# Kernel tuning notes

Measured on AMD Instinct MI355X. Metric: run time of the kernel, lower is better.

## Reference

```python
import jax, jax.numpy as jnp
import numpy as np

S = 16384   # total tokens (batch*seq flattened)
D = 1024    # model_dim
E = 32      # num_global_experts
H = 1024    # expert hidden size
CAP = 512   # capacity = capacity_factor * ceil(S / E)


def setup_inputs() -> dict:
    key = jax.random.key(0)
    k1, k2, k3, k4 = jax.random.split(key, 4)
    x = jax.random.normal(k1, (S, D), jnp.float32)
    wg = jax.random.normal(k2, (E, D), jnp.float32) * 0.02
    w1 = jax.random.normal(k3, (E, D, H), jnp.float32) * 0.02
    w2 = jax.random.normal(k4, (E, H, D), jnp.float32) * 0.02
    return {"x": x, "wg": wg, "w1": w1, "w2": w2}


def _moe_forward(x, wg, w1, w2):
    # --- Top1Gate ---
    logits = x @ wg.T                                   # [S, E]
    gates = jax.nn.softmax(logits, axis=1)              # [S, E]
    idx = jnp.argmax(logits, axis=1)                    # [S] int
    mask1 = jax.nn.one_hot(idx, E, dtype=jnp.int32)     # [S, E]
    gates1_s = jnp.sum(gates * mask1.astype(gates.dtype), axis=1)  # [S]
    # load-balance aux loss (fp32 path)
    me = jnp.sum(gates.astype(jnp.float32), axis=0)
    ce = jnp.sum(mask1.astype(jnp.float32), axis=0)
    l_loss = jnp.sum(me * ce) * (float(E) / float(S * S))
    # positions within expert (tutel cumsum_sub_one)
    loc = jnp.sum(jnp.cumsum(mask1, axis=0) * mask1, axis=1) - 1   # [S]
    valid = loc < CAP                                   # capacity drop
    slot = jnp.where(valid, idx * CAP + loc, 0)         # flat slot id, dropped -> 0 (masked below)

    # --- GatingEncoder: scatter tokens into [E*CAP, D] buffer ---
    xm = x * valid[:, None].astype(x.dtype)
    dispatched = jnp.zeros((E * CAP, D), x.dtype).at[slot].add(xm)
    dispatched = dispatched.reshape(E, CAP, D)

    # --- ExpertsGemm: per-expert FFN (world_size == 1, all-to-all is identity) ---
    h = jax.nn.relu(jnp.einsum('ecd,edh->ech', dispatched, w1))    # [E, CAP, H]
    expert_out = jnp.einsum('ech,ehd->ecd', h, w2).reshape(E * CAP, D)

    # --- GatingDecoder: gather back + weight by gate ---
    y = expert_out[slot] * (gates1_s * valid.astype(gates1_s.dtype))[:, None]
    return y, l_loss


def reference(x, wg, w1, w2):
    return _moe_forward(x, wg, w1, w2)
```

## Files before the change

kernel.cpp:

```cpp
#include <hip/hip_runtime.h>
#include <stdint.h>

static constexpr int nS   = 16384;
static constexpr int nD   = 1024;
static constexpr int nE   = 32;
static constexpr int nH   = 1024;
static constexpr int nCAP = 512;

static constexpr int GT = 64;
static constexpr int GB = nS / GT;

typedef __bf16 bf16x8 __attribute__((ext_vector_type(8)));
typedef float  f32x4  __attribute__((ext_vector_type(4)));
typedef unsigned short u16x8 __attribute__((ext_vector_type(8)));

static __device__ __forceinline__ unsigned short f2bf(float f) {
    __bf16 h = (__bf16)f;
    return __builtin_bit_cast(unsigned short, h);
}

static __device__ __forceinline__ void gload16(const void* g, void* l) {
    __builtin_amdgcn_global_load_lds(
        (const __attribute__((address_space(1))) void*)g,
        (__attribute__((address_space(3))) void*)l, 16, 0, 0);
}

__global__ __launch_bounds__(128) void k_gate(
    const float* __restrict__ x, const float* __restrict__ wg,
    unsigned short* __restrict__ xbf, int* __restrict__ idxo,
    float* __restrict__ gateval, int* __restrict__ counts,
    float* __restrict__ me_part)
{
    __shared__ float xs[GT][65];
    __shared__ float wgs[nE][65];
    __shared__ float gl[GT][nE + 1];
    __shared__ int   hist[nE];

    const int tid = threadIdx.x;
    const int tb  = blockIdx.x * GT;
    if (tid < nE) hist[tid] = 0;

    const int t0 = (tid >> 3) * 4;
    const int e0 = (tid & 7) * 4;
    float acc[4][4] = {};

    for (int ch = 0; ch < nD / 64; ++ch) {
#pragma unroll
        for (int i = 0; i < 4; ++i) {
            int f = tid + i * 128;
            int r = f >> 4, c4 = f & 15;
            const float4 v = *(const float4*)&wg[(size_t)r * nD + ch * 64 + c4 * 4];
            wgs[r][c4*4+0] = v.x; wgs[r][c4*4+1] = v.y;
            wgs[r][c4*4+2] = v.z; wgs[r][c4*4+3] = v.w;
        }
#pragma unroll
        for (int i = 0; i < 8; ++i) {
            int f = tid + i * 128;
            int r = f >> 4, c4 = f & 15;
            size_t go = (size_t)(tb + r) * nD + ch * 64 + c4 * 4;
            const float4 v = *(const float4*)&x[go];
            xs[r][c4*4+0] = v.x; xs[r][c4*4+1] = v.y;
            xs[r][c4*4+2] = v.z; xs[r][c4*4+3] = v.w;
            unsigned long long pk = (unsigned long long)f2bf(v.x)
                | ((unsigned long long)f2bf(v.y) << 16)
                | ((unsigned long long)f2bf(v.z) << 32)
                | ((unsigned long long)f2bf(v.w) << 48);
            *(unsigned long long*)&xbf[go] = pk;
        }
        __syncthreads();
#pragma unroll 4
        for (int k = 0; k < 64; ++k) {
            float xa[4], wb[4];
#pragma unroll
            for (int i = 0; i < 4; ++i) xa[i] = xs[t0 + i][k];
#pragma unroll
            for (int j = 0; j < 4; ++j) wb[j] = wgs[e0 + j][k];
#pragma unroll
            for (int i = 0; i < 4; ++i)
#pragma unroll
                for (int j = 0; j < 4; ++j) acc[i][j] += xa[i] * wb[j];
        }
        __syncthreads();
    }

#pragma unroll
    for (int i = 0; i < 4; ++i)
#pragma unroll
        for (int j = 0; j < 4; ++j) gl[t0 + i][e0 + j] = acc[i][j];
    __syncthreads();

    if (tid < GT) {
        float mx = gl[tid][0]; int bi = 0;
#pragma unroll
        for (int e = 1; e < nE; ++e) { float v = gl[tid][e]; if (v > mx) { mx = v; bi = e; } }
        float den = 0.f;
#pragma unroll
        for (int e = 0; e < nE; ++e) { float g = expf(gl[tid][e] - mx); gl[tid][e] = g; den += g; }
        float inv = 1.f / den;
#pragma unroll
        for (int e = 0; e < nE; ++e) gl[tid][e] *= inv;
        idxo[tb + tid] = bi;
        gateval[tb + tid] = inv;
        atomicAdd(&hist[bi], 1);
    }
    __syncthreads();
    if (tid < nE) {
        float s = 0.f;
        for (int t = 0; t < GT; ++t) s += gl[t][tid];
        me_part[blockIdx.x * nE + tid] = s;
        counts[blockIdx.x * nE + tid] = hist[tid];
    }
}

__global__ __launch_bounds__(1024) void k_scan(
    const int* __restrict__ counts, int* __restrict__ offsets,
    const float* __restrict__ me_part, float* __restrict__ loss_out,
    int* __restrict__ inv_slot)
{
    __shared__ int tot[nE];
    __shared__ float mesum[nE];
    const int w = threadIdx.x >> 6;
    const int lane = threadIdx.x & 63;
    for (int e = w; e < nE; e += 16) {
        int v[4]; int s = 0;
#pragma unroll
        for (int i = 0; i < 4; ++i) { v[i] = counts[(lane * 4 + i) * nE + e]; s += v[i]; }
        int incl = s;
#pragma unroll
        for (int d = 1; d < 64; d <<= 1) {
            int o = __shfl_up(incl, d);
            if (lane >= d) incl += o;
        }
        int run = incl - s;
#pragma unroll
        for (int i = 0; i < 4; ++i) { offsets[(lane * 4 + i) * nE + e] = run; run += v[i]; }
        int total = __shfl(incl, 63);
        if (lane == 0) tot[e] = total;

        float ms = 0.f;
#pragma unroll
        for (int i = 0; i < 4; ++i) ms += me_part[(lane * 4 + i) * nE + e];
#pragma unroll
        for (int d = 32; d >= 1; d >>= 1) ms += __shfl_xor(ms, d);
        if (lane == 0) mesum[e] = ms;
    }
    __syncthreads();
    if (threadIdx.x < 64) {
        float val = (threadIdx.x < nE) ? mesum[threadIdx.x] * (float)tot[threadIdx.x] : 0.f;
#pragma unroll
        for (int d = 32; d >= 1; d >>= 1) val += __shfl_xor(val, d);
        if (threadIdx.x == 0)
            *loss_out = val * ((float)nE / ((float)nS * (float)nS));
    }
    for (int i = threadIdx.x; i < nE * nCAP; i += 1024) {
        const int e = i >> 9, loc = i & (nCAP - 1);
        if (loc >= tot[e]) inv_slot[i] = -1;
    }
}

__global__ __launch_bounds__(64) void k_assign(
    const int* __restrict__ idxi, const int* __restrict__ offsets,
    int* __restrict__ inv_slot, float* __restrict__ y)
{
    __shared__ int drop[64];
    __shared__ int ndrop;
    const int lane = threadIdx.x;
    const int t = blockIdx.x * 64 + lane;
    const int e = idxi[t];
    if (lane == 0) ndrop = 0;
    __syncthreads();
    int rank = 0;
#pragma unroll
    for (int ee = 0; ee < nE; ++ee) {
        unsigned long long m = __ballot(e == ee);
        if (e == ee) rank = __popcll(m & ((1ull << lane) - 1ull));
    }
    const int loc = offsets[blockIdx.x * nE + e] + rank;
    if (loc < nCAP) {
        inv_slot[e * nCAP + loc] = t;
    } else {
        int p = atomicAdd(&ndrop, 1);
        drop[p] = t;
    }
    __syncthreads();
    const int nd = ndrop;
    for (int i = 0; i < nd; ++i) {
        const int tt = drop[i];
        float4 z = {0.f, 0.f, 0.f, 0.f};
        for (int c = lane; c < nD / 4; c += 64)
            *(float4*)&y[(size_t)tt * nD + c * 4] = z;
    }
}

__global__ __launch_bounds__(256) void k_transpose(
    const float* __restrict__ w1, const float* __restrict__ w2,
    unsigned short* __restrict__ w1t, unsigned short* __restrict__ w2t)
{
    __shared__ unsigned short T[64 * 258];
    const float* src = blockIdx.z ? w2 : w1;
    unsigned short* dst = blockIdx.z ? w2t : w1t;
    const int e    = blockIdx.y;
    const int dblk = blockIdx.x & 15;
    const int hblk = blockIdx.x >> 4;
    const int t = threadIdx.x;
    const int wv = t >> 6, lane = t & 63;

    const float* sbase = src + ((size_t)e * 1024 + dblk * 64) * 1024 + hblk * 256;

#pragma unroll
    for (int i = 0; i < 16; ++i) {
        const int d = i * 4 + wv;
        const float4 v = *(const float4*)&sbase[(size_t)d * 1024 + lane * 4];
        unsigned long long pk = (unsigned long long)f2bf(v.x)
            | ((unsigned long long)f2bf(v.y) << 16)
            | ((unsigned long long)f2bf(v.z) << 32)
            | ((unsigned long long)f2bf(v.w) << 48);
        *(unsigned long long*)&T[d * 258 + lane * 4] = pk;
    }
    __syncthreads();

    const size_t cbase0 = (((size_t)e * 8 + hblk * 2) * 16 + dblk) * 8192;
    const size_t cbase1 = cbase0 + 16 * 8192;
#pragma unroll
    for (int s = 0; s < 8; ++s) {
        const int off = s * 2048 + t * 8;
        const int hl  = off >> 6;
        const int k8  = off & 63;
        u16x8 v;
#pragma unroll
        for (int r = 0; r < 8; ++r) v[r] = T[(k8 + r) * 258 + hl];
        const size_t base = (off < 8192) ? cbase0 : cbase1;
        *(u16x8*)&dst[base + (off & 8191)] = v;
    }
}

template <int MODE>
__global__ __launch_bounds__(256) void k_gemm(
    const unsigned short* __restrict__ Abase,
    const unsigned short* __restrict__ Bt,
    const int* __restrict__ inv_slot,
    const float* __restrict__ gateval,
    unsigned short* __restrict__ hout,
    float* __restrict__ y)
{
    __shared__ __attribute__((aligned(16))) unsigned short As[128 * 64];
    __shared__ __attribute__((aligned(16))) unsigned short Bs[128 * 64];

    const int tid = threadIdx.x;
    const int lane = tid & 63, w = tid >> 6;
    const int n0 = blockIdx.x * 128, m0 = blockIdx.y * 128, e = blockIdx.z;

    const unsigned short* gA[4];
    const int j = lane & 7;
#pragma unroll
    for (int s = 0; s < 4; ++s) {
        const int cw = s * 4 + w;
        const int row = cw * 8 + (lane >> 3);
        if (MODE == 0) {
            int tok = inv_slot[e * nCAP + m0 + row];
            if (tok < 0) tok = 0;
            gA[s] = Abase + (size_t)tok * nD + j * 8;
        } else {
            gA[s] = Abase + ((size_t)e * nCAP + m0 + row) * nH + j * 8;
        }
    }
    const unsigned short* gB = Bt + (((size_t)e * 8 + (n0 >> 7)) * 16) * 8192
                             + (size_t)tid * 8;

    f32x4 acc[4][4];
#pragma unroll
    for (int a = 0; a < 4; ++a)
#pragma unroll
        for (int b = 0; b < 4; ++b) acc[a][b] = (f32x4){0.f, 0.f, 0.f, 0.f};

    const int wm = w >> 1, wn = w & 1;
    const int abyte = (wm * 64 + (lane & 15)) * 128 + (lane >> 4) * 16;
    const int bbyte = (wn * 64 + (lane & 15)) * 128 + (lane >> 4) * 16;

    for (int k0 = 0; k0 < 1024 / 64; ++k0) {
#pragma unroll
        for (int s = 0; s < 4; ++s) {
            gload16(gA[s] + k0 * 64, (char*)As + (s * 4 + w) * 1024);
            gload16(gB + (size_t)k0 * 8192 + ((s * 4 + w) * 512 + lane * 8 - tid * 8),
                    (char*)Bs + (s * 4 + w) * 1024);
        }
        __syncthreads();
#pragma unroll
        for (int kk = 0; kk < 2; ++kk) {
            bf16x8 a[4], b[4];
#pragma unroll
            for (int mi = 0; mi < 4; ++mi)
                a[mi] = *(const bf16x8*)((const char*)As + abyte + mi * 2048 + kk * 64);
#pragma unroll
            for (int ni = 0; ni < 4; ++ni)
                b[ni] = *(const bf16x8*)((const char*)Bs + bbyte + ni * 2048 + kk * 64);
#pragma unroll
            for (int mi = 0; mi < 4; ++mi)
#pragma unroll
                for (int ni = 0; ni < 4; ++ni)
                    acc[mi][ni] = __builtin_amdgcn_mfma_f32_16x16x32_bf16(
                        a[mi], b[ni], acc[mi][ni], 0, 0, 0);
        }
        __syncthreads();
    }

    const int col_l = lane & 15, rg = lane >> 4;
    if (MODE == 0) {
#pragma unroll
        for (int mi = 0; mi < 4; ++mi) {
#pragma unroll
            for (int ni = 0; ni < 4; ++ni) {
                const f32x4 v = acc[mi][ni];
                const int n = n0 + wn * 64 + ni * 16 + col_l;
#pragma unroll
                for (int r = 0; r < 4; ++r) {
                    const int m = m0 + wm * 64 + mi * 16 + rg * 4 + r;
                    const float f = v[r] > 0.f ? v[r] : 0.f;
                    hout[((size_t)e * nCAP + m) * nH + n] = f2bf(f);
                }
            }
        }
    } else {
#pragma unroll
        for (int mi = 0; mi < 4; ++mi) {
            int tok[4]; float gv[4];
#pragma unroll
            for (int r = 0; r < 4; ++r) {
                const int m = m0 + wm * 64 + mi * 16 + rg * 4 + r;
                tok[r] = inv_slot[e * nCAP + m];
                gv[r] = (tok[r] >= 0) ? gateval[tok[r]] : 0.f;
            }
#pragma unroll
            for (int ni = 0; ni < 4; ++ni) {
                const f32x4 v = acc[mi][ni];
                const int n = n0 + wn * 64 + ni * 16 + col_l;
#pragma unroll
                for (int r = 0; r < 4; ++r) {
                    if (tok[r] >= 0)
                        y[(size_t)tok[r] * nD + n] = v[r] * gv[r];
                }
            }
        }
    }
}

extern "C" void kernel_launch(void* const* d_in, const int* in_sizes, int n_in,
                              void* d_out, int out_size, void* d_ws, size_t ws_size,
                              hipStream_t stream) {
    const float* x  = (const float*)d_in[0];
    const float* wg = (const float*)d_in[1];
    const float* w1 = (const float*)d_in[2];
    const float* w2 = (const float*)d_in[3];
    float* y = (float*)d_out;
    float* loss = y + (size_t)nS * nD;

    char* ws = (char*)d_ws;
    unsigned short* w1t  = (unsigned short*)(ws);
    unsigned short* w2t  = (unsigned short*)(ws + (64ull << 20));
    unsigned short* hbuf = (unsigned short*)(ws + (128ull << 20));
    unsigned short* xbf  = (unsigned short*)(ws + (160ull << 20));
    char* p = ws + (192ull << 20);
    int*   idxb    = (int*)p;   p += (size_t)nS * 4;
    float* gateval = (float*)p; p += (size_t)nS * 4;
    int*   counts  = (int*)p;   p += (size_t)GB * nE * 4;
    int*   offsets = (int*)p;   p += (size_t)GB * nE * 4;
    float* me_part = (float*)p; p += (size_t)GB * nE * 4;
    int*   inv_slot= (int*)p;

    k_gate<<<GB, 128, 0, stream>>>(x, wg, xbf, idxb, gateval, counts, me_part);
    k_scan<<<1, 1024, 0, stream>>>(counts, offsets, me_part, loss, inv_slot);
    k_assign<<<GB, 64, 0, stream>>>(idxb, offsets, inv_slot, y);
    k_transpose<<<dim3(64, 32, 2), 256, 0, stream>>>(w1, w2, w1t, w2t);
    k_gemm<0><<<dim3(8, 4, 32), 256, 0, stream>>>(xbf, w1t, inv_slot, gateval, hbuf, y);
    k_gemm<1><<<dim3(8, 4, 32), 256, 0, stream>>>(hbuf, w2t, inv_slot, gateval, hbuf, y);
}
```

Measured before the change: 311.2 us.

## Stage GEMM epilogues through LDS for coalesced stores and remap blocks per XCD

Both GEMM epilogues now write the accumulator tile into shared memory first and then store it with 16-byte vectorized rows. Before, each thread issued scattered 2-byte (bf16) or 4-byte (fp32) stores. The y scatter in the second GEMM now writes contiguous float4 chunks per token row, done in two halves so the fp32 tile fits in LDS. Launch is flattened to 1024 blocks with a swizzled block-id so that consecutive blocks landing on the same XCD share an expert, which should improve L2 reuse of weights. The cost is extra LDS traffic and barriers in the epilogue.

Measured after the change: 312.0 us. About the same (+0.2%).

```diff
diff --git a/kernel.cpp b/kernel.cpp
--- a/kernel.cpp
+++ b/kernel.cpp
@@ -243,12 +243,14 @@
     unsigned short* __restrict__ hout,
     float* __restrict__ y)
 {
-    __shared__ __attribute__((aligned(16))) unsigned short As[128 * 64];
-    __shared__ __attribute__((aligned(16))) unsigned short Bs[128 * 64];
+    __shared__ __attribute__((aligned(16))) unsigned short SMEM[128 * 64 * 2];
+    unsigned short* As = SMEM;
+    unsigned short* Bs = SMEM + 128 * 64;
 
     const int tid = threadIdx.x;
     const int lane = tid & 63, w = tid >> 6;
-    const int n0 = blockIdx.x * 128, m0 = blockIdx.y * 128, e = blockIdx.z;
+    const int bid = (blockIdx.x & 7) * 128 + (blockIdx.x >> 3);
+    const int n0 = (bid & 7) * 128, m0 = ((bid >> 3) & 3) * 128, e = bid >> 5;
 
     const unsigned short* gA[4];
     const int j = lane & 7;
@@ -311,35 +313,56 @@
 #pragma unroll
             for (int ni = 0; ni < 4; ++ni) {
                 const f32x4 v = acc[mi][ni];
-                const int n = n0 + wn * 64 + ni * 16 + col_l;
+                const int nl = wn * 64 + ni * 16 + col_l;
 #pragma unroll
                 for (int r = 0; r < 4; ++r) {
-                    const int m = m0 + wm * 64 + mi * 16 + rg * 4 + r;
+                    const int ml = wm * 64 + mi * 16 + rg * 4 + r;
                     const float f = v[r] > 0.f ? v[r] : 0.f;
-                    hout[((size_t)e * nCAP + m) * nH + n] = f2bf(f);
+                    SMEM[ml * 128 + nl] = f2bf(f);
                 }
             }
         }
+        __syncthreads();
+#pragma unroll
+        for (int s = 0; s < 8; ++s) {
+            const int u = tid + s * 256;
+            const int row = u >> 4, nu = u & 15;
+            const u16x8 v = *(const u16x8*)((const char*)SMEM + u * 16);
+            *(u16x8*)&hout[((size_t)e * nCAP + m0 + row) * nH + n0 + nu * 8] = v;
+        }
     } else {
-#pragma unroll
-        for (int mi = 0; mi < 4; ++mi) {
-            int tok[4]; float gv[4];
-#pragma unroll
-            for (int r = 0; r < 4; ++r) {
-                const int m = m0 + wm * 64 + mi * 16 + rg * 4 + r;
-                tok[r] = inv_slot[e * nCAP + m];
-                gv[r] = (tok[r] >= 0) ? gateval[tok[r]] : 0.f;
-            }
-#pragma unroll
-            for (int ni = 0; ni < 4; ++ni) {
-                const f32x4 v = acc[mi][ni];
-                const int n = n0 + wn * 64 + ni * 16 + col_l;
-#pragma unroll
-                for (int r = 0; r < 4; ++r) {
-                    if (tok[r] >= 0)
-                        y[(size_t)tok[r] * nD + n] = v[r] * gv[r];
+        float* Lf = (float*)SMEM;
+#pragma unroll
+        for (int P = 0; P < 2; ++P) {
+            if (wm == P) {
+#pragma unroll
+                for (int mi = 0; mi < 4; ++mi) {
+#pragma unroll
+                    for (int ni = 0; ni < 4; ++ni) {
+                        const f32x4 v = acc[mi][ni];
+                        const int nl = wn * 64 + ni * 16 + col_l;
+#pragma unroll
+                        for (int r = 0; r < 4; ++r) {
+                            const int ml = mi * 16 + rg * 4 + r;
+                            Lf[ml * 128 + nl] = v[r];
+                        }
+                    }
                 }
             }
+            __syncthreads();
+#pragma unroll
+            for (int s = 0; s < 8; ++s) {
+                const int u = tid + s * 256;
+                const int row = u >> 5, f4 = u & 31;
+                const int tok = inv_slot[e * nCAP + m0 + P * 64 + row];
+                if (tok >= 0) {
+                    const float gv = gateval[tok];
+                    float4 v = *(const float4*)((const char*)SMEM + u * 16);
+                    v.x *= gv; v.y *= gv; v.z *= gv; v.w *= gv;
+                    *(float4*)&y[(size_t)tok * nD + n0 + f4 * 4] = v;
+                }
+            }
+            __syncthreads();
         }
     }
 }
@@ -371,6 +394,6 @@
     k_scan<<<1, 1024, 0, stream>>>(counts, offsets, me_part, loss, inv_slot);
     k_assign<<<GB, 64, 0, stream>>>(idxb, offsets, inv_slot, y);
     k_transpose<<<dim3(64, 32, 2), 256, 0, stream>>>(w1, w2, w1t, w2t);
-    k_gemm<0><<<dim3(8, 4, 32), 256, 0, stream>>>(xbf, w1t, inv_slot, gateval, hbuf, y);
-    k_gemm<1><<<dim3(8, 4, 32), 256, 0, stream>>>(hbuf, w2t, inv_slot, gateval, hbuf, y);
-}
+    k_gemm<0><<<1024, 256, 0, stream>>>(xbf, w1t, inv_slot, gateval, hbuf, y);
+    k_gemm<1><<<1024, 256, 0, stream>>>(hbuf, w2t, inv_slot, gateval, hbuf, y);
+}
```
